# Optimization experiments

Measured on AMD Instinct MI355X. Metric: run time of the kernel, lower is better.

## Reference

```python
import jax, jax.numpy as jnp
import numpy as np

DIM = 512
NUM_HEADS = 8
EXPAND = 3
D1 = EXPAND * DIM          # 1536, divisible by NUM_HEADS
HEAD_DIM = D1 // NUM_HEADS  # 192
RPE_DIM = 64
RPE_LAYERS = 3
GLU_DIM = 1024
GAMMA = 0.999
EPS = 1e-8


def srms(x):
    # SimpleRMSNorm: x / (||x||_2 / sqrt(d) + eps), parameter-free
    d = x.shape[-1]
    rms = jnp.linalg.norm(x, axis=-1, keepdims=True) * (d ** -0.5)
    return x / (rms + EPS)


def setup_inputs() -> dict:
    key = jax.random.key(0)
    ks = jax.random.split(key, 12)
    def w(k, shape):
        return jax.random.normal(k, shape, dtype=jnp.float32) * 0.02
    B, H, W = 16, 32, 32
    return {
        "x": jax.random.normal(ks[0], (B, H * W, DIM), dtype=jnp.float32),
        "u_w": w(ks[1], (DIM, D1)), "u_b": jnp.zeros((D1,), jnp.float32),
        "v_w": w(ks[2], (DIM, D1)), "v_b": jnp.zeros((D1,), jnp.float32),
        "o_w": w(ks[3], (D1, DIM)), "o_b": jnp.zeros((DIM,), jnp.float32),
        "pos_w": w(ks[4], (2, RPE_DIM)), "pos_b": jnp.zeros((RPE_DIM,), jnp.float32),
        "rpe_lw": w(ks[5], (RPE_LAYERS, RPE_DIM, RPE_DIM)),
        "rpe_lb": jnp.zeros((RPE_LAYERS, RPE_DIM), jnp.float32),
        "rpe_ow": w(ks[6], (RPE_DIM, NUM_HEADS * HEAD_DIM)),
        "rpe_ob": jnp.zeros((NUM_HEADS * HEAD_DIM,), jnp.float32),
        "l1_w": w(ks[7], (DIM, GLU_DIM)), "l1_b": jnp.zeros((GLU_DIM,), jnp.float32),
        "l2_w": w(ks[8], (DIM, GLU_DIM)), "l2_b": jnp.zeros((GLU_DIM,), jnp.float32),
        "l3_w": w(ks[9], (GLU_DIM, DIM)), "l3_b": jnp.zeros((DIM,), jnp.float32),
        "H": H, "W": W,
    }


def _rpe(pos, pos_w, pos_b, rpe_lw, rpe_lb, rpe_ow, rpe_ob):
    # pos: (P, 2) relative 2D offsets -> (P, NUM_HEADS*HEAD_DIM) Toeplitz coefficients
    x = pos @ pos_w + pos_b
    for i in range(RPE_LAYERS):  # norm -> act -> linear
        x = jax.nn.silu(srms(x)) @ rpe_lw[i] + rpe_lb[i]
    return jax.nn.silu(srms(x)) @ rpe_ow + rpe_ob


def _gtu2d(x, H, W, u_w, u_b, v_w, v_b, o_w, o_b,
           pos_w, pos_b, rpe_lw, rpe_lb, rpe_ow, rpe_ob):
    B, N, _ = x.shape
    u = jax.nn.silu(x @ u_w + u_b)                 # (B, N, D1)
    v = jax.nn.silu(x @ v_w + v_b)                 # (B, N, D1)
    v = v.reshape(B, H, W, NUM_HEADS, HEAD_DIM).transpose(0, 3, 1, 2, 4)  # b h H W d
    # circular layout of relative offsets for FFT lengths (2H, 2W):
    # index a in [0, 2H) maps to offset a if a < H else a - 2H
    di = jnp.concatenate([jnp.arange(H), jnp.arange(-H, 0)]).astype(jnp.float32)
    dj = jnp.concatenate([jnp.arange(W), jnp.arange(-W, 0)]).astype(jnp.float32)
    pos = jnp.stack(jnp.meshgrid(di, dj, indexing="ij"), axis=-1)  # (2H, 2W, 2)
    coef = _rpe(pos.reshape(-1, 2), pos_w, pos_b, rpe_lw, rpe_lb, rpe_ow, rpe_ob)
    coef = coef.reshape(2 * H, 2 * W, NUM_HEADS, HEAD_DIM).transpose(2, 0, 1, 3)  # h 2H 2W d
    # decay mask gamma^(|di|+|dj|)
    decay = GAMMA ** (jnp.abs(di)[:, None] + jnp.abs(dj)[None, :])  # (2H, 2W)
    coef = coef * decay[None, :, :, None]
    # block-Toeplitz token mixing as 2D circular convolution via FFT
    vf = jnp.fft.rfft2(v, s=(2 * H, 2 * W), axes=(2, 3))
    cf = jnp.fft.rfft2(coef, s=(2 * H, 2 * W), axes=(1, 2))
    out = jnp.fft.irfft2(vf * cf[None], s=(2 * H, 2 * W), axes=(2, 3))[:, :, :H, :W, :]
    out = out.transpose(0, 2, 3, 1, 4).reshape(B, N, D1)
    return (u * out) @ o_w + o_b


def reference(x, u_w, u_b, v_w, v_b, o_w, o_b, pos_w, pos_b,
              rpe_lw, rpe_lb, rpe_ow, rpe_ob,
              l1_w, l1_b, l2_w, l2_b, l3_w, l3_b, H, W):
    x = x + _gtu2d(x, H, W, u_w, u_b, v_w, v_b, o_w, o_b,
                   pos_w, pos_b, rpe_lw, rpe_lb, rpe_ow, rpe_ob)
    mlp = (jax.nn.silu(x @ l1_w + l1_b) * (x @ l2_w + l2_b)) @ l3_w + l3_b
    return x + srms(mlp)
```

## Files before the change

kernel.cpp:

```cpp
#include <hip/hip_runtime.h>
#include <math.h>

#define B_   16
#define NN   1024
#define DIM_ 512
#define D1_  1536
#define GLU_ 1024

typedef unsigned short u16;
typedef __attribute__((ext_vector_type(8))) short bf16x8;
typedef __attribute__((ext_vector_type(4))) float f32x4;

__device__ __forceinline__ float silu_f(float x) {
    return x / (1.0f + __expf(-x));
}
__device__ __forceinline__ u16 f2b(float f) {
    unsigned u = __float_as_uint(f);
    return (u16)((u + 0x7FFF + ((u >> 16) & 1)) >> 16);
}
__device__ __forceinline__ float b2f(u16 s) {
    return __uint_as_float(((unsigned)s) << 16);
}

__launch_bounds__(256)
__global__ void prep_kernel(const float* __restrict__ x, u16* __restrict__ xb,
                            const float* __restrict__ u_w, u16* __restrict__ uwT,
                            const float* __restrict__ v_w, u16* __restrict__ vwT,
                            const float* __restrict__ o_w, u16* __restrict__ owT,
                            const float* __restrict__ l1_w, const float* __restrict__ l2_w,
                            u16* __restrict__ gluT,
                            const float* __restrict__ l3_w, u16* __restrict__ l3T,
                            const float* __restrict__ rpe_ow, u16* __restrict__ owT2,
                            const float* __restrict__ l1_b, const float* __restrict__ l2_b,
                            float* __restrict__ gluB,
                            const float* __restrict__ pos_w, const float* __restrict__ pos_b,
                            const float* __restrict__ lw, const float* __restrict__ lb,
                            u16* __restrict__ y) {
    __shared__ __align__(16) char smem_raw[4352];
    int bb = blockIdx.x;
    int t = threadIdx.x;
    if (bb < 2048) {
        #pragma unroll
        for (int j = 0; j < 4; ++j) {
            int i = bb * 1024 + j * 256 + t;
            float4 f = reinterpret_cast<const float4*>(x)[i];
            unsigned lo = (unsigned)f2b(f.x) | ((unsigned)f2b(f.y) << 16);
            unsigned hi = (unsigned)f2b(f.z) | ((unsigned)f2b(f.w) << 16);
            reinterpret_cast<uint2*>(xb)[i] = make_uint2(lo, hi);
        }
    } else if (bb < 5984) {
        const float* in; u16* out; int K, N, tile;
        if (bb < 2816)      { in = u_w;  out = uwT;  K = 512;  N = 1536; tile = bb - 2048; }
        else if (bb < 3584) { in = v_w;  out = vwT;  K = 512;  N = 1536; tile = bb - 2816; }
        else if (bb < 4352) { in = o_w;  out = owT;  K = 1536; N = 512;  tile = bb - 3584; }
        else if (bb < 4864) { in = l1_w; out = gluT; K = 512;  N = 1024; tile = bb - 4352; }
        else if (bb < 5376) { in = l2_w; out = gluT + (size_t)GLU_ * DIM_; K = 512; N = 1024; tile = bb - 4864; }
        else if (bb < 5888) { in = l3_w; out = l3T;  K = 1024; N = 512;  tile = bb - 5376; }
        else                { in = rpe_ow; out = owT2; K = 64; N = 1536; tile = bb - 5888; }
        float (*tl)[33] = (float(*)[33])smem_raw;
        int tiles_x = N >> 5;
        int n0 = (tile % tiles_x) * 32, k0 = (tile / tiles_x) * 32;
        int tx = t & 31, ty = t >> 5;
        #pragma unroll
        for (int r = 0; r < 32; r += 8)
            tl[ty + r][tx] = in[(size_t)(k0 + ty + r) * N + n0 + tx];
        __syncthreads();
        #pragma unroll
        for (int r = 0; r < 32; r += 8)
            out[(size_t)(n0 + ty + r) * K + k0 + tx] = f2b(tl[tx][ty + r]);
    } else if (bb < 5992) {
        int i = (bb - 5984) * 256 + t;
        gluB[i] = (i < 1024) ? l1_b[i] : l2_b[i - 1024];
    } else {
        float (*yb)[64] = (float(*)[64])smem_raw;
        int lane = t & 63;
        int wv = t >> 6;
        int a = (bb - 5992) * 4 + wv;
        int a1 = a >> 6, a2 = a & 63;
        float di = (a1 < 32) ? (float)a1 : (float)(a1 - 64);
        float dj = (a2 < 32) ? (float)a2 : (float)(a2 - 64);
        float xv = di * pos_w[lane] + dj * pos_w[64 + lane] + pos_b[lane];
        for (int L = 0; L < 3; ++L) {
            float ss = xv * xv;
            #pragma unroll
            for (int o = 32; o > 0; o >>= 1) ss += __shfl_xor(ss, o, 64);
            float yv = silu_f(xv / (sqrtf(ss) * 0.125f + 1e-8f));
            yb[wv][lane] = yv;
            __syncthreads();
            float acc = lb[L * 64 + lane];
            const float* w = lw + L * 4096 + lane;
            #pragma unroll 8
            for (int k = 0; k < 64; ++k) acc = fmaf(yb[wv][k], w[k * 64], acc);
            __syncthreads();
            xv = acc;
        }
        float ss = xv * xv;
        #pragma unroll
        for (int o = 32; o > 0; o >>= 1) ss += __shfl_xor(ss, o, 64);
        float yv = silu_f(xv / (sqrtf(ss) * 0.125f + 1e-8f));
        y[(size_t)a * 64 + lane] = f2b(yv);
    }
}

template<int EPI, int PERMB>
__launch_bounds__(256, 4)
__global__ void mfma_gemm(const u16* __restrict__ A, const u16* __restrict__ BT,
                          const float* __restrict__ bias, const float* __restrict__ R,
                          void* __restrict__ C0, void* __restrict__ C1,
                          int M, int N, int K) {
    __shared__ __align__(16) u16 Asmem[128 * 64];
    __shared__ __align__(16) u16 Bsmem[128 * 64];
    int nwg = gridDim.x * gridDim.y;
    int bid = blockIdx.y * gridDim.x + blockIdx.x;
    int qq = nwg >> 3, rr = nwg & 7;
    int xcd = bid & 7, lid = bid >> 3;
    int swz = (xcd < rr ? xcd * (qq + 1) : rr * (qq + 1) + (xcd - rr) * qq) + lid;
    int bx = swz % gridDim.x, by = swz / gridDim.x;
    int tid = threadIdx.x;
    int w = tid >> 6, lane = tid & 63;
    int lr = lane & 15, kg = lane >> 4;
    int wr = w >> 1, wc = w & 1;
    int m0 = by * 128, n0 = bx * 128;
    f32x4 acc[4][4] = {};
    for (int k0 = 0; k0 < K; k0 += 64) {
        #pragma unroll
        for (int r = 0; r < 4; ++r) {
            int c4 = (r * 4 + w) * 64 + lane;
            int row = c4 >> 3, slot = c4 & 7;
            int sl = slot ^ (row & 7);
            const u16* ga = A + (size_t)(m0 + row) * K + k0 + sl * 8;
            int grow = n0 + row;
            if (PERMB == 1) {
                grow = (grow & ~1023) | ((grow & 31) << 5) | ((grow >> 5) & 31);
            } else if (PERMB == 2) {
                int c = grow & 127;
                int f = ((grow >> 7) << 6) + ((c >> 6) << 5) + (((c >> 5) & 1) << 4) + (c & 15);
                grow = (((c >> 4) & 1) << 10) + f;
            } else if (PERMB == 3) {
                grow = ((grow & 63) << 6) | ((grow >> 6) & 63);
            }
            const u16* gb = BT + (size_t)grow * K + k0 + sl * 8;
            u16* la = Asmem + (r * 4 + w) * 512;
            u16* lb = Bsmem + (r * 4 + w) * 512;
            __builtin_amdgcn_global_load_lds((const __attribute__((address_space(1))) void*)ga,
                                             (__attribute__((address_space(3))) void*)la, 16, 0, 0);
            __builtin_amdgcn_global_load_lds((const __attribute__((address_space(1))) void*)gb,
                                             (__attribute__((address_space(3))) void*)lb, 16, 0, 0);
        }
        __syncthreads();
        #pragma unroll
        for (int kk = 0; kk < 2; ++kk) {
            bf16x8 af[4], bfr[4];
            #pragma unroll
            for (int m = 0; m < 4; ++m) {
                int row = wr * 64 + m * 16 + lr;
                int sl = (kk * 4 + kg) ^ (row & 7);
                af[m] = *reinterpret_cast<const bf16x8*>(&Asmem[row * 64 + sl * 8]);
            }
            #pragma unroll
            for (int n = 0; n < 4; ++n) {
                int row = wc * 64 + n * 16 + lr;
                int sl = (kk * 4 + kg) ^ (row & 7);
                bfr[n] = *reinterpret_cast<const bf16x8*>(&Bsmem[row * 64 + sl * 8]);
            }
            #pragma unroll
            for (int m = 0; m < 4; ++m)
                #pragma unroll
                for (int n = 0; n < 4; ++n)
                    acc[m][n] = __builtin_amdgcn_mfma_f32_16x16x32_bf16(af[m], bfr[n], acc[m][n], 0, 0, 0);
        }
        __syncthreads();
    }
    if (EPI == 5) {
        #pragma unroll
        for (int m = 0; m < 4; ++m) {
            #pragma unroll
            for (int np = 0; np < 2; ++np) {
                int n = np * 2;
                int f = (n0 >> 1) + wc * 32 + np * 16 + lr;
                #pragma unroll
                for (int q = 0; q < 4; ++q) {
                    int row = m0 + wr * 64 + m * 16 + kg * 4 + q;
                    float a1 = acc[m][n][q] + bias[f];
                    float a2 = acc[m][n + 1][q] + bias[1024 + f];
                    ((u16*)C0)[(size_t)row * GLU_ + f] = f2b(silu_f(a1) * a2);
                }
            }
        }
    } else {
        #pragma unroll
        for (int m = 0; m < 4; ++m) {
            #pragma unroll
            for (int n = 0; n < 4; ++n) {
                #pragma unroll
                for (int q = 0; q < 4; ++q) {
                    int row = m0 + wr * 64 + m * 16 + kg * 4 + q;
                    int col = n0 + wc * 64 + n * 16 + lr;
                    size_t idx = (size_t)row * N + col;
                    if (EPI == 0) {
                        float vv = acc[m][n][q] + bias[col];
                        ((u16*)C0)[idx] = f2b(silu_f(vv));
                    } else if (EPI == 1) {
                        ((u16*)C0)[idx] = f2b(acc[m][n][q] + bias[col] + R[idx]);
                    } else if (EPI == 2) {
                        ((u16*)C0)[idx] = f2b(acc[m][n][q] + bias[col]);
                    } else if (EPI == 4) {
                        float vv = acc[m][n][q] + bias[row];
                        ((u16*)C0)[idx] = f2b(silu_f(vv));
                    } else {
                        int dii = col & 63, djj = (col >> 6) & 63;
                        float adi = (dii < 32) ? (float)dii : (float)(64 - dii);
                        float adj = (djj < 32) ? (float)djj : (float)(64 - djj);
                        float decay = __expf(-0.0010005003335835344f * (adi + adj));
                        ((u16*)C0)[idx] = f2b((acc[m][n][q] + bias[row]) * decay);
                    }
                }
            }
        }
    }
}

__launch_bounds__(512, 1)
__global__ void conv_mfma_kernel(const u16* __restrict__ coefTT, const u16* __restrict__ vT2,
                                 u16* __restrict__ mixT) {
    __shared__ __align__(16) u16 vlds[16384];
    __shared__ __align__(16) u16 gt[32768];
    __shared__ __align__(16) u16 d2l[4096];
    int c = blockIdx.x;
    int t = threadIdx.x;
    int wv = t >> 6, lane = t & 63;
    int lr = lane & 15, kg = lane >> 4;
    int lrs = lr & 7;

    int mbc[4];
    #pragma unroll
    for (int nt = 0; nt < 4; ++nt)
        mbc[nt] = (((kg * 8 - (nt * 8 + wv)) & 63) & ~7) >> 3;

    #pragma unroll
    for (int pass = 0; pass < 4; ++pass) {
        int L = pass * 512 + t;
        int b = L >> 7, k8s = L & 127;
        int k8 = k8s ^ (b & 7);
        const u16* src = vT2 + (size_t)c * 16384 + b * 1024 + k8 * 8;
        u16* dst = vlds + (size_t)(pass * 512 + wv * 64) * 8;
        __builtin_amdgcn_global_load_lds((const __attribute__((address_space(1))) void*)src,
                                         (__attribute__((address_space(3))) void*)dst, 16, 0, 0);
    }
    {
        const u16* src = coefTT + (size_t)c * 4096 + t * 8;
        u16* dst = d2l + wv * 512;
        __builtin_amdgcn_global_load_lds((const __attribute__((address_space(1))) void*)src,
                                         (__attribute__((address_space(3))) void*)dst, 16, 0, 0);
    }
    __syncthreads();

    for (int e = t; e < 32768; e += 512) {
        int m = e & 63, w = (e >> 6) & 63, o = e >> 12;
        int oo = (8 - o) & 7;
        int q = (64 - ((m + oo) & 63)) & 63;
        gt[(o * 64 + w) * 64 + ((m >> 3) ^ (w & 7)) * 8 + (m & 7)] = d2l[w * 64 + q];
    }
    __syncthreads();

    f32x4 acc[4][2] = {};
    const bf16x8* vb8 = (const bf16x8*)vlds;
    const bf16x8* gtw = (const bf16x8*)gt + wv * 512;
    for (int jp = 0; jp < 32; ++jp) {
        bf16x8 af = vb8[lr * 128 + ((jp * 4 + kg) ^ lrs)];
        int w0 = (lr - jp) & 63;
        int w1 = (w0 + 16) & 63;
        #pragma unroll
        for (int nt = 0; nt < 4; ++nt) {
            bf16x8 b0 = gtw[w0 * 8 + (mbc[nt] ^ (w0 & 7))];
            acc[nt][0] = __builtin_amdgcn_mfma_f32_16x16x32_bf16(af, b0, acc[nt][0], 0, 0, 0);
            bf16x8 b1 = gtw[w1 * 8 + (mbc[nt] ^ (w1 & 7))];
            acc[nt][1] = __builtin_amdgcn_mfma_f32_16x16x32_bf16(af, b1, acc[nt][1], 0, 0, 0);
        }
    }
    __syncthreads();

    #pragma unroll
    for (int nt = 0; nt < 4; ++nt) {
        #pragma unroll
        for (int h = 0; h < 2; ++h) {
            int p = nt * 256 + wv * 32 + h * 16 + lr;
            #pragma unroll
            for (int q = 0; q < 4; ++q) {
                int b = kg * 4 + q;
                vlds[b * 1024 + (p ^ ((b & 7) << 3))] = f2b(acc[nt][h][q]);
            }
        }
    }
    __syncthreads();

    const uint4* src16 = (const uint4*)vlds;
    #pragma unroll
    for (int pass = 0; pass < 4; ++pass) {
        int L = pass * 512 + t;
        int b = L >> 7;
        int pc = (L & 127) ^ (b & 7);
        uint4 val = src16[L];
        *reinterpret_cast<uint4*>(mixT + (size_t)c * 16384 + b * 1024 + pc * 8) = val;
    }
}

__launch_bounds__(256)
__global__ void mult_kernel(const u16* __restrict__ mixT, u16* __restrict__ u) {
    int r = blockIdx.x * 256 + threadIdx.x;
    int c0 = blockIdx.y * 64;
    #pragma unroll
    for (int oc = 0; oc < 8; ++oc) {
        int cb = c0 + oc * 8;
        float mv[8];
        #pragma unroll
        for (int m2 = 0; m2 < 8; ++m2)
            mv[m2] = b2f(mixT[(size_t)(cb + m2) * 16384 + r]);
        u16 uv[8];
        *reinterpret_cast<uint4*>(uv) = *reinterpret_cast<const uint4*>(&u[(size_t)r * D1_ + cb]);
        #pragma unroll
        for (int m2 = 0; m2 < 8; ++m2) uv[m2] = f2b(b2f(uv[m2]) * mv[m2]);
        *reinterpret_cast<uint4*>(&u[(size_t)r * D1_ + cb]) = *reinterpret_cast<uint4*>(uv);
    }
}

__launch_bounds__(256)
__global__ void final_kernel(const u16* __restrict__ x2b, const u16* __restrict__ m,
                             float* __restrict__ out) {
    int row = blockIdx.x;
    const u16* mr = m + (size_t)row * DIM_;
    const u16* xr = x2b + (size_t)row * DIM_;
    float* orow = out + (size_t)row * DIM_;
    int t = threadIdx.x;
    float a = b2f(mr[t]), b2 = b2f(mr[t + 256]);
    float ss = a * a + b2 * b2;
    #pragma unroll
    for (int o = 32; o > 0; o >>= 1) ss += __shfl_xor(ss, o, 64);
    __shared__ float red[4];
    int wid = t >> 6;
    if ((t & 63) == 0) red[wid] = ss;
    __syncthreads();
    float tot = red[0] + red[1] + red[2] + red[3];
    float inv = 1.0f / (sqrtf(tot) * 0.044194173824159216f + 1e-8f);
    orow[t]       = b2f(xr[t])       + a  * inv;
    orow[t + 256] = b2f(xr[t + 256]) + b2 * inv;
}

extern "C" void kernel_launch(void* const* d_in, const int* in_sizes, int n_in,
                              void* d_out, int out_size, void* d_ws, size_t ws_size,
                              hipStream_t stream) {
    const float* x     = (const float*)d_in[0];
    const float* u_w   = (const float*)d_in[1];
    const float* u_b   = (const float*)d_in[2];
    const float* v_w   = (const float*)d_in[3];
    const float* v_b   = (const float*)d_in[4];
    const float* o_w   = (const float*)d_in[5];
    const float* o_b   = (const float*)d_in[6];
    const float* pos_w = (const float*)d_in[7];
    const float* pos_b = (const float*)d_in[8];
    const float* rpe_lw = (const float*)d_in[9];
    const float* rpe_lb = (const float*)d_in[10];
    const float* rpe_ow = (const float*)d_in[11];
    const float* rpe_ob = (const float*)d_in[12];
    const float* l1_w  = (const float*)d_in[13];
    const float* l1_b  = (const float*)d_in[14];
    const float* l2_w  = (const float*)d_in[15];
    const float* l2_b  = (const float*)d_in[16];
    const float* l3_w  = (const float*)d_in[17];
    const float* l3_b  = (const float*)d_in[18];
    float* out = (float*)d_out;

    u16* coefTT = (u16*)d_ws;
    u16* xb     = coefTT + 6291456;
    u16* u      = xb + 8388608;
    u16* vT2    = u + 25165824;
    u16* mixT   = vT2 + 25165824;
    u16* x2b    = mixT + 25165824;
    u16* uwT    = x2b + 8388608;
    u16* vwT    = uwT + 786432;
    u16* owT    = vwT + 786432;
    u16* gluT   = owT + 786432;
    u16* l3T    = gluT + 1048576;
    float* gluB = (float*)(l3T + 524288);
    u16* y      = (u16*)(gluB + 2048);
    u16* owT2   = y + 262144;
    u16* p      = u;
    u16* mm     = vT2;

    const int M = B_ * NN;

    prep_kernel<<<7016, 256, 0, stream>>>(x, xb, u_w, uwT, v_w, vwT, o_w, owT,
                                          l1_w, l2_w, gluT, l3_w, l3T, rpe_ow, owT2,
                                          l1_b, l2_b, gluB, pos_w, pos_b, rpe_lw, rpe_lb, y);
    mfma_gemm<6, 3><<<dim3(4096 / 128, D1_ / 128), 256, 0, stream>>>(owT2, y, rpe_ob, nullptr, coefTT, nullptr, D1_, 4096, 64);
    mfma_gemm<4, 1><<<dim3(M / 128, D1_ / 128), 256, 0, stream>>>(vwT, xb, v_b, nullptr, vT2, nullptr, D1_, M, DIM_);
    conv_mfma_kernel<<<1536, 512, 0, stream>>>(coefTT, vT2, mixT);
    mfma_gemm<0, 0><<<dim3(D1_ / 128, M / 128), 256, 0, stream>>>(xb, uwT, u_b, nullptr, u, nullptr, M, D1_, DIM_);
    mult_kernel<<<dim3(M / 256, D1_ / 64), 256, 0, stream>>>(mixT, u);
    mfma_gemm<1, 0><<<dim3(DIM_ / 128, M / 128), 256, 0, stream>>>(u, owT, o_b, x, x2b, nullptr, M, DIM_, D1_);
    mfma_gemm<5, 2><<<dim3(2 * GLU_ / 128, M / 128), 256, 0, stream>>>(x2b, gluT, gluB, nullptr, p, nullptr, M, 2 * GLU_, DIM_);
    mfma_gemm<2, 0><<<dim3(DIM_ / 128, M / 128), 256, 0, stream>>>(p, l3T, l3_b, nullptr, mm, nullptr, M, DIM_, GLU_);
    final_kernel<<<M, 256, 0, stream>>>(x2b, mm, out);
}
```

Measured before the change: 369.0 us.

## Fuse mix multiply into u GEMM epilogue and pre-rotate conv coefficients

Removes the separate mult_kernel by multiplying the conv output into the silu(u) GEMM epilogue, which avoids a read-modify-write pass over the u tensor. The coefficient GEMM now writes a pre-rotated, padded layout (72-wide rows with an 8-element wrap). This lets the conv kernel build its shifted LDS table with vectorized 16-byte reads and selects instead of a scalar gather. The residual read in the out-projection switches from the fp32 x to the bf16 xb, which halves that traffic but adds rounding error to the residual path.

```diff
diff --git a/kernel.cpp b/kernel.cpp
--- a/kernel.cpp
+++ b/kernel.cpp
@@ -105,8 +105,8 @@
 template<int EPI, int PERMB>
 __launch_bounds__(256, 4)
 __global__ void mfma_gemm(const u16* __restrict__ A, const u16* __restrict__ BT,
-                          const float* __restrict__ bias, const float* __restrict__ R,
-                          void* __restrict__ C0, void* __restrict__ C1,
+                          const float* __restrict__ bias, const void* __restrict__ R,
+                          void* __restrict__ C0, const void* __restrict__ C1,
                           int M, int N, int K) {
     __shared__ __align__(16) u16 Asmem[128 * 64];
     __shared__ __align__(16) u16 Bsmem[128 * 64];
@@ -187,6 +187,24 @@
                 }
             }
         }
+    } else if (EPI == 7) {
+        const u16* mixT = (const u16*)C1;
+        #pragma unroll
+        for (int m = 0; m < 4; ++m) {
+            #pragma unroll
+            for (int n = 0; n < 4; ++n) {
+                int rowbase = m0 + wr * 64 + m * 16 + kg * 4;
+                int col = n0 + wc * 64 + n * 16 + lr;
+                u16 mv[4];
+                *reinterpret_cast<uint2*>(mv) =
+                    *reinterpret_cast<const uint2*>(&mixT[(size_t)col * 16384 + rowbase]);
+                #pragma unroll
+                for (int q = 0; q < 4; ++q) {
+                    float vv = acc[m][n][q] + bias[col];
+                    ((u16*)C0)[(size_t)(rowbase + q) * N + col] = f2b(silu_f(vv) * b2f(mv[q]));
+                }
+            }
+        }
     } else {
         #pragma unroll
         for (int m = 0; m < 4; ++m) {
@@ -201,7 +219,7 @@
                         float vv = acc[m][n][q] + bias[col];
                         ((u16*)C0)[idx] = f2b(silu_f(vv));
                     } else if (EPI == 1) {
-                        ((u16*)C0)[idx] = f2b(acc[m][n][q] + bias[col] + R[idx]);
+                        ((u16*)C0)[idx] = f2b(acc[m][n][q] + bias[col] + b2f(((const u16*)R)[idx]));
                     } else if (EPI == 2) {
                         ((u16*)C0)[idx] = f2b(acc[m][n][q] + bias[col]);
                     } else if (EPI == 4) {
@@ -212,7 +230,11 @@
                         float adi = (dii < 32) ? (float)dii : (float)(64 - dii);
                         float adj = (djj < 32) ? (float)djj : (float)(64 - djj);
                         float decay = __expf(-0.0010005003335835344f * (adi + adj));
-                        ((u16*)C0)[idx] = f2b((acc[m][n][q] + bias[row]) * decay);
+                        u16 val = f2b((acc[m][n][q] + bias[row]) * decay);
+                        int s = (64 - dii) & 63;
+                        size_t base = (size_t)row * 4608 + djj * 72;
+                        ((u16*)C0)[base + s] = val;
+                        if (s < 8) ((u16*)C0)[base + s + 64] = val;
                     }
                 }
             }
@@ -221,11 +243,11 @@
 }
 
 __launch_bounds__(512, 1)
-__global__ void conv_mfma_kernel(const u16* __restrict__ coefTT, const u16* __restrict__ vT2,
+__global__ void conv_mfma_kernel(const u16* __restrict__ coefR, const u16* __restrict__ vT2,
                                  u16* __restrict__ mixT) {
     __shared__ __align__(16) u16 vlds[16384];
     __shared__ __align__(16) u16 gt[32768];
-    __shared__ __align__(16) u16 d2l[4096];
+    __shared__ __align__(16) u16 d2l[4608];
     int c = blockIdx.x;
     int t = threadIdx.x;
     int wv = t >> 6, lane = t & 63;
@@ -248,18 +270,43 @@
                                          (__attribute__((address_space(3))) void*)dst, 16, 0, 0);
     }
     {
-        const u16* src = coefTT + (size_t)c * 4096 + t * 8;
+        const u16* src = coefR + (size_t)c * 4608 + t * 8;
         u16* dst = d2l + wv * 512;
         __builtin_amdgcn_global_load_lds((const __attribute__((address_space(1))) void*)src,
                                          (__attribute__((address_space(3))) void*)dst, 16, 0, 0);
     }
+    if (wv == 0) {
+        const u16* src = coefR + (size_t)c * 4608 + (512 + lane) * 8;
+        u16* dst = d2l + 4096;
+        __builtin_amdgcn_global_load_lds((const __attribute__((address_space(1))) void*)src,
+                                         (__attribute__((address_space(3))) void*)dst, 16, 0, 0);
+    }
     __syncthreads();
 
-    for (int e = t; e < 32768; e += 512) {
-        int m = e & 63, w = (e >> 6) & 63, o = e >> 12;
-        int oo = (8 - o) & 7;
-        int q = (64 - ((m + oo) & 63)) & 63;
-        gt[(o * 64 + w) * 64 + ((m >> 3) ^ (w & 7)) * 8 + (m & 7)] = d2l[w * 64 + q];
+    {
+        const bf16x8* d2l8 = (const bf16x8*)d2l;
+        bf16x8* gt8 = (bf16x8*)gt;
+        int oo = (8 - wv) & 7;
+        #pragma unroll
+        for (int j = 0; j < 8; ++j) {
+            int ci = j * 64 + lane;
+            int w = ci >> 3, m8s = ci & 7;
+            int m8 = m8s ^ (w & 7);
+            bf16x8 A = d2l8[w * 9 + m8];
+            bf16x8 Bn = d2l8[w * 9 + m8 + 1];
+            u16 av[16], ov[8];
+            *reinterpret_cast<bf16x8*>(av) = A;
+            *reinterpret_cast<bf16x8*>(av + 8) = Bn;
+            #pragma unroll
+            for (int e = 0; e < 8; ++e) {
+                u16 r = av[e];
+                #pragma unroll
+                for (int s2 = 1; s2 < 8; ++s2)
+                    r = (oo == s2) ? av[e + s2] : r;
+                ov[e] = r;
+            }
+            gt8[wv * 512 + ci] = *reinterpret_cast<bf16x8*>(ov);
+        }
     }
     __syncthreads();
 
@@ -302,25 +349,6 @@
         int pc = (L & 127) ^ (b & 7);
         uint4 val = src16[L];
         *reinterpret_cast<uint4*>(mixT + (size_t)c * 16384 + b * 1024 + pc * 8) = val;
-    }
-}
-
-__launch_bounds__(256)
-__global__ void mult_kernel(const u16* __restrict__ mixT, u16* __restrict__ u) {
-    int r = blockIdx.x * 256 + threadIdx.x;
-    int c0 = blockIdx.y * 64;
-    #pragma unroll
-    for (int oc = 0; oc < 8; ++oc) {
-        int cb = c0 + oc * 8;
-        float mv[8];
-        #pragma unroll
-        for (int m2 = 0; m2 < 8; ++m2)
-            mv[m2] = b2f(mixT[(size_t)(cb + m2) * 16384 + r]);
-        u16 uv[8];
-        *reinterpret_cast<uint4*>(uv) = *reinterpret_cast<const uint4*>(&u[(size_t)r * D1_ + cb]);
-        #pragma unroll
-        for (int m2 = 0; m2 < 8; ++m2) uv[m2] = f2b(b2f(uv[m2]) * mv[m2]);
-        *reinterpret_cast<uint4*>(&u[(size_t)r * D1_ + cb]) = *reinterpret_cast<uint4*>(uv);
     }
 }
 
@@ -370,8 +398,8 @@
     const float* l3_b  = (const float*)d_in[18];
     float* out = (float*)d_out;
 
-    u16* coefTT = (u16*)d_ws;
-    u16* xb     = coefTT + 6291456;
+    u16* coefR  = (u16*)d_ws;
+    u16* xb     = coefR + 7077888;
     u16* u      = xb + 8388608;
     u16* vT2    = u + 25165824;
     u16* mixT   = vT2 + 25165824;
@@ -392,12 +420,11 @@
     prep_kernel<<<7016, 256, 0, stream>>>(x, xb, u_w, uwT, v_w, vwT, o_w, owT,
                                           l1_w, l2_w, gluT, l3_w, l3T, rpe_ow, owT2,
                                           l1_b, l2_b, gluB, pos_w, pos_b, rpe_lw, rpe_lb, y);
-    mfma_gemm<6, 3><<<dim3(4096 / 128, D1_ / 128), 256, 0, stream>>>(owT2, y, rpe_ob, nullptr, coefTT, nullptr, D1_, 4096, 64);
+    mfma_gemm<6, 3><<<dim3(4096 / 128, D1_ / 128), 256, 0, stream>>>(owT2, y, rpe_ob, nullptr, coefR, nullptr, D1_, 4096, 64);
     mfma_gemm<4, 1><<<dim3(M / 128, D1_ / 128), 256, 0, stream>>>(vwT, xb, v_b, nullptr, vT2, nullptr, D1_, M, DIM_);
-    conv_mfma_kernel<<<1536, 512, 0, stream>>>(coefTT, vT2, mixT);
-    mfma_gemm<0, 0><<<dim3(D1_ / 128, M / 128), 256, 0, stream>>>(xb, uwT, u_b, nullptr, u, nullptr, M, D1_, DIM_);
-    mult_kernel<<<dim3(M / 256, D1_ / 64), 256, 0, stream>>>(mixT, u);
-    mfma_gemm<1, 0><<<dim3(DIM_ / 128, M / 128), 256, 0, stream>>>(u, owT, o_b, x, x2b, nullptr, M, DIM_, D1_);
+    conv_mfma_kernel<<<1536, 512, 0, stream>>>(coefR, vT2, mixT);
+    mfma_gemm<7, 0><<<dim3(D1_ / 128, M / 128), 256, 0, stream>>>(xb, uwT, u_b, nullptr, u, mixT, M, D1_, DIM_);
+    mfma_gemm<1, 0><<<dim3(DIM_ / 128, M / 128), 256, 0, stream>>>(u, owT, o_b, xb, x2b, nullptr, M, DIM_, D1_);
     mfma_gemm<5, 2><<<dim3(2 * GLU_ / 128, M / 128), 256, 0, stream>>>(x2b, gluT, gluB, nullptr, p, nullptr, M, 2 * GLU_, DIM_);
     mfma_gemm<2, 0><<<dim3(DIM_ / 128, M / 128), 256, 0, stream>>>(p, l3T, l3_b, nullptr, mm, nullptr, M, DIM_, GLU_);
     final_kernel<<<M, 256, 0, stream>>>(x2b, mm, out);
```

Result: faster. 328.8 us (-10.9%).
